# Performance work log

Measured on AMD Instinct MI355X. Metric: run time of the kernel, lower is better.

The kernel has to match this reference:

```python
import jax, jax.numpy as jnp
import numpy as np

N, T, D, H, NH, BS = 4, 4096, 512, 8, 4, 64
DH = D // H                 # head dim = 64
NB = T // BS                # n_buckets = 64
CS = NH * NB                # chunk_size = 256
L = NH * T                  # sorted sequence length per head


def setup_inputs() -> dict:
    key = jax.random.key(0)
    ks = jax.random.split(key, 4)
    x = jax.random.normal(ks[0], (N, T, D), jnp.float32)
    W_Q = jax.random.normal(ks[1], (D, D), jnp.float32) * (D ** -0.5)
    W_V = jax.random.normal(ks[2], (D, D), jnp.float32) * (D ** -0.5)
    b_Q = jnp.zeros((D,), jnp.float32)
    b_V = jnp.zeros((D,), jnp.float32)
    gamma = jnp.ones((D,), jnp.float32)
    beta = jnp.zeros((D,), jnp.float32)
    # per-head random rotations: (dim_head, num_hashes, n_buckets // 2)
    rotations = jax.random.normal(ks[3], (H, DH, NH, NB // 2), jnp.float32)
    return {"x": x, "W_Q": W_Q, "b_Q": b_Q, "W_V": W_V, "b_V": b_V,
            "gamma": gamma, "beta": beta, "rotations": rotations}


def _look_one_back(a):
    # concat each chunk with the previous chunk (wrap-around for chunk 0)
    extra = jnp.concatenate([a[:, -1:], a[:, :-1]], axis=1)
    return jnp.concatenate([a, extra], axis=2)


def _lsh_head(qk, v, rot):
    # qk, v: [N, T, DH]; rot: [DH, NH, NB//2]
    rotated = jnp.einsum('btf,fhi->bhti', qk, rot)               # [N,NH,T,NB//2]
    rotated = jnp.concatenate([rotated, -rotated], axis=-1)       # [N,NH,T,NB]
    buckets = jnp.argmax(rotated, axis=-1)                        # [N,NH,T]
    offsets = (jnp.arange(NH) * NB)[None, :, None]
    buckets = (buckets + offsets).reshape(N, L)                   # [N, NH*T]

    ticker = jnp.broadcast_to(jnp.arange(L)[None, :], (N, L))
    buckets_and_t = T * buckets + (ticker % T)                    # unique keys
    sticker = jnp.argsort(buckets_and_t, axis=-1)                 # sorted ticker ids
    undo_sort = jnp.argsort(sticker, axis=-1)
    st = sticker % T                                              # original positions

    sqk = jnp.take_along_axis(qk, st[..., None], axis=1)          # [N,L,DH]
    sv = jnp.take_along_axis(v, st[..., None], axis=1)

    bq_t = st.reshape(N, CS, -1)                                  # [N,CS,BS]
    bqk = sqk.reshape(N, CS, -1, DH)
    bv = sv.reshape(N, CS, -1, DH)
    bq = bqk
    bk = bqk / (jnp.linalg.norm(bqk, axis=-1, keepdims=True) + 1e-6)

    bk = _look_one_back(bk)                                       # [N,CS,2*BS,DH]
    bv = _look_one_back(bv)
    bkv_t = _look_one_back(bq_t)

    dots = jnp.einsum('bcie,bcje->bcij', bq, bk) * (DH ** -0.5)   # [N,CS,BS,2BS]

    # mask out pairs hashed to different buckets
    q_sb = jnp.take_along_axis(buckets, sticker, axis=1).reshape(N, CS, -1)
    kv_sb = _look_one_back(q_sb)
    dots = jnp.where(q_sb[:, :, :, None] != kv_sb[:, :, None, :], -1e9, dots)
    # down-weight self-attention (same position)
    dots = jnp.where(bq_t[:, :, :, None] == bkv_t[:, :, None, :], -1e-5, dots)

    lse = jax.nn.logsumexp(dots, axis=-1, keepdims=True)
    probs = jnp.exp(dots - lse)
    bo = jnp.einsum('bcij,bcje->bcie', probs, bv)                 # [N,CS,BS,DH]

    so = bo.reshape(N, L, DH)
    slog = lse.reshape(N, L)
    o = jnp.take_along_axis(so, undo_sort[..., None], axis=1)
    logits = jnp.take_along_axis(slog, undo_sort, axis=1)

    o = o.reshape(N, NH, T, DH)
    logits = logits.reshape(N, NH, T, 1)
    pw = jnp.exp(logits - jax.nn.logsumexp(logits, axis=1, keepdims=True))
    return jnp.sum(o * pw, axis=1)                                # [N,T,DH]


def reference(x, W_Q, b_Q, W_V, b_V, gamma, beta, rotations):
    Q = x @ W_Q + b_Q
    V = x @ W_V + b_V
    Qh = Q.reshape(N, T, H, DH).transpose(2, 0, 1, 3)             # [H,N,T,DH]
    Vh = V.reshape(N, T, H, DH).transpose(2, 0, 1, 3)
    outs = jax.vmap(_lsh_head)(Qh, Vh, rotations)                 # [H,N,T,DH]
    out = outs.transpose(1, 2, 0, 3).reshape(N, T, D)
    mu = out.mean(axis=-1, keepdims=True)
    var = out.var(axis=-1, keepdims=True)
    return gamma * (out - mu) / jnp.sqrt(var + 1e-3) + beta
```

## Files before the change

kernel.cpp:

```cpp
#include <hip/hip_runtime.h>
#include <hip/hip_bf16.h>

#define N_ 4
#define T_ 4096
#define D_ 512
#define H_ 8
#define DH_ 64
#define NH_ 4
#define NB_ 64
#define CS_ 256
#define L_ 16384

typedef unsigned short u16;
typedef unsigned int u32;
typedef __attribute__((ext_vector_type(8))) short short8;
typedef __attribute__((ext_vector_type(8))) _Float16 half8;
typedef __attribute__((ext_vector_type(4))) float f32x4;

__device__ __forceinline__ u16 f2bf(float x){
    union { float f; u32 u; } c; c.f = x;
    u32 u = c.u;
    u32 r = (u + 0x7FFFu + ((u >> 16) & 1u)) >> 16;
    return (u16)r;
}
__device__ __forceinline__ float bf2f(u16 b){
    union { u32 u; float f; } c; c.u = ((u32)b) << 16;
    return c.f;
}
__device__ __forceinline__ u16 f2h(float x){
    _Float16 h = (_Float16)x;
    u16 r; __builtin_memcpy(&r, &h, 2); return r;
}

__global__ __launch_bounds__(256) void k_decXf(const float* __restrict__ x,
        u16* __restrict__ xf){
    int i = blockIdx.x * 256 + threadIdx.x;
    float4 v = ((const float4*)x)[i];
    ushort4 o;
    o.x = f2h(v.x); o.y = f2h(v.y); o.z = f2h(v.z); o.w = f2h(v.w);
    ((ushort4*)xf)[i] = o;
}

__global__ __launch_bounds__(256) void k_decWv(const float* __restrict__ Wv,
        u16* __restrict__ wvt){
    __shared__ float tile[32][33];
    const int tid = threadIdx.x;
    const int kt = blockIdx.x * 32, nt = blockIdx.y * 32;
    const int tx = tid & 31, ty = tid >> 5;
    #pragma unroll
    for (int i = 0; i < 4; ++i)
        tile[ty + i * 8][tx] = Wv[(size_t)(kt + ty + i * 8) * 512 + nt + tx];
    __syncthreads();
    #pragma unroll
    for (int i = 0; i < 4; ++i){
        int n = ty + i * 8;
        wvt[(size_t)(nt + n) * 512 + kt + tx] = f2h(tile[tx][n]);
    }
}

__global__ __launch_bounds__(256) void k_q(const float* __restrict__ x,
        const float* __restrict__ Wq, const float* __restrict__ bq,
        float* __restrict__ Q, u16* __restrict__ Qbf, float* __restrict__ qinv){
    __shared__ float sA[16][132];
    __shared__ float sB[16][68];
    const int tid = threadIdx.x;
    const int tx = tid & 15, ty = tid >> 4;
    const int mb = blockIdx.x * 128, nb = blockIdx.y * 64;
    const int h = blockIdx.y;
    float acc[8][4] = {};
    for (int k0 = 0; k0 < 512; k0 += 16){
        #pragma unroll
        for (int i = 0; i < 2; ++i){
            int idx = i * 256 + tid;
            int m = idx >> 2, kq = idx & 3;
            float4 v = *(const float4*)&x[(size_t)(mb + m) * 512 + k0 + kq * 4];
            sA[kq * 4 + 0][m] = v.x;
            sA[kq * 4 + 1][m] = v.y;
            sA[kq * 4 + 2][m] = v.z;
            sA[kq * 4 + 3][m] = v.w;
        }
        {
            int kk = tid >> 4, nq = tid & 15;
            *(float4*)&sB[kk][nq * 4] =
                *(const float4*)&Wq[(size_t)(k0 + kk) * 512 + nb + nq * 4];
        }
        __syncthreads();
        #pragma unroll
        for (int kk = 0; kk < 16; ++kk){
            float a[8], b[4];
            *(float4*)&a[0] = *(const float4*)&sA[kk][ty * 8];
            *(float4*)&a[4] = *(const float4*)&sA[kk][ty * 8 + 4];
            *(float4*)&b[0] = *(const float4*)&sB[kk][tx * 4];
            #pragma unroll
            for (int i = 0; i < 8; ++i)
                #pragma unroll
                for (int j = 0; j < 4; ++j) acc[i][j] += a[i] * b[j];
        }
        __syncthreads();
    }
    float4 bi = *(const float4*)&bq[nb + tx * 4];
    #pragma unroll
    for (int i = 0; i < 8; ++i){
        float o0 = acc[i][0] + bi.x, o1 = acc[i][1] + bi.y;
        float o2 = acc[i][2] + bi.z, o3 = acc[i][3] + bi.w;
        int m = mb + ty * 8 + i;
        float4 o4; o4.x = o0; o4.y = o1; o4.z = o2; o4.w = o3;
        *(float4*)&Q[(size_t)m * 512 + nb + tx * 4] = o4;
        float ss = o0 * o0 + o1 * o1 + o2 * o2 + o3 * o3;
        #pragma unroll
        for (int s = 8; s >= 1; s >>= 1) ss += __shfl_xor(ss, s, 64);
        int n = m >> 12, t = m & (T_ - 1);
        size_t rowb = (size_t)(h * N_ + n) * T_ + t;
        if (tx == 0) qinv[rowb] = 1.f / (sqrtf(ss) + 1e-6f);
        ushort4 ob;
        ob.x = f2bf(o0); ob.y = f2bf(o1); ob.z = f2bf(o2); ob.w = f2bf(o3);
        *(ushort4*)&Qbf[rowb * 64 + tx * 4] = ob;
    }
}

__global__ __launch_bounds__(256) void k_gemmV(const u16* __restrict__ xf,
        const u16* __restrict__ wvt, const float* __restrict__ bv,
        u16* __restrict__ Vbf){
    __shared__ __align__(16) u16 sA[128 * 40];
    __shared__ __align__(16) u16 sB[128 * 40];
    const int tid = threadIdx.x;
    const int mb = blockIdx.x * 128, nb = blockIdx.y * 128;
    const int w = tid >> 6, lane = tid & 63, quad = lane >> 4, cc = lane & 15;
    const int wm = (w & 1) * 64, wn = (w >> 1) * 64;
    f32x4 acc[4][4];
    #pragma unroll
    for (int i = 0; i < 4; ++i)
        #pragma unroll
        for (int j = 0; j < 4; ++j) acc[i][j] = (f32x4){0.f, 0.f, 0.f, 0.f};

    for (int k0 = 0; k0 < 512; k0 += 32){
        #pragma unroll
        for (int i = 0; i < 2; ++i){
            int idx = i * 256 + tid;
            int m = idx >> 2, ks = idx & 3;
            *(short8*)&sA[m * 40 + ks * 8] =
                *(const short8*)&xf[(size_t)(mb + m) * 512 + k0 + ks * 8];
            *(short8*)&sB[m * 40 + ks * 8] =
                *(const short8*)&wvt[(size_t)(nb + m) * 512 + k0 + ks * 8];
        }
        __syncthreads();
        half8 a[4], b[4];
        #pragma unroll
        for (int i = 0; i < 4; ++i){
            a[i] = *(const half8*)&sA[(wm + i * 16 + cc) * 40 + quad * 8];
            b[i] = *(const half8*)&sB[(wn + i * 16 + cc) * 40 + quad * 8];
        }
        #pragma unroll
        for (int i = 0; i < 4; ++i)
            #pragma unroll
            for (int j = 0; j < 4; ++j)
                acc[i][j] = __builtin_amdgcn_mfma_f32_16x16x32_f16(a[i], b[j], acc[i][j], 0, 0, 0);
        __syncthreads();
    }
    #pragma unroll
    for (int i = 0; i < 4; ++i)
        #pragma unroll
        for (int j = 0; j < 4; ++j){
            int c = nb + wn + j * 16 + cc;
            int hh = c >> 6, d = c & 63;
            float bi = bv[c];
            #pragma unroll
            for (int r = 0; r < 4; ++r){
                int m = mb + wm + i * 16 + quad * 4 + r;
                int n = m >> 12, t = m & (T_ - 1);
                Vbf[((size_t)(hh * N_ + n) * T_ + t) * 64 + d] = f2bf(acc[i][j][r] + bi);
            }
        }
}

__global__ __launch_bounds__(256) void k_rot(const float* __restrict__ Q,
        const float* __restrict__ rot, int* __restrict__ buckets){
    const int tb = blockIdx.x * 32;
    const int n = blockIdx.y, h = blockIdx.z;
    const int hn = h * N_ + n;
    __shared__ float Rs[64 * 128];
    __shared__ float Qs[32][64];
    const int tid = threadIdx.x;
    const float* rh = rot + (size_t)h * (64 * 128);
    for (int i = tid; i < 8192; i += 256) Rs[i] = rh[i];
    for (int i = tid; i < 2048; i += 256){
        int t = i >> 6, f = i & 63;
        Qs[t][f] = Q[(size_t)(n * T_ + tb + t) * 512 + h * 64 + f];
    }
    __syncthreads();
    const int tx = tid & 31, tg = tid >> 5;
    float r[4][4] = {};
    for (int f = 0; f < 64; ++f){
        float q0 = Qs[tg * 4 + 0][f], q1 = Qs[tg * 4 + 1][f];
        float q2 = Qs[tg * 4 + 2][f], q3 = Qs[tg * 4 + 3][f];
        #pragma unroll
        for (int jj = 0; jj < 4; ++jj){
            float rv = Rs[f * 128 + jj * 32 + tx];
            r[0][jj] += q0 * rv; r[1][jj] += q1 * rv;
            r[2][jj] += q2 * rv; r[3][jj] += q3 * rv;
        }
    }
    #pragma unroll
    for (int tt = 0; tt < 4; ++tt){
        #pragma unroll
        for (int jj = 0; jj < 4; ++jj){
            float bv = r[tt][jj]; int bi = tx;
            float nv = -bv;
            if (nv > bv){ bv = nv; bi = 32 + tx; }
            #pragma unroll
            for (int m = 16; m >= 1; m >>= 1){
                float ov = __shfl_xor(bv, m, 32);
                int   oi = __shfl_xor(bi, m, 32);
                if (ov > bv || (ov == bv && oi < bi)){ bv = ov; bi = oi; }
            }
            if (tx == 0){
                int t = tb + tg * 4 + tt;
                buckets[(size_t)hn * L_ + jj * T_ + t] = bi + jj * 64;
            }
        }
    }
}

__global__ __launch_bounds__(256) void k_hist(const int* __restrict__ buckets,
        int* __restrict__ hist){
    const int tile = blockIdx.x, hn = blockIdx.y;
    const int tid = threadIdx.x;
    __shared__ int h[256];
    h[tid] = 0;
    __syncthreads();
    int b = buckets[(size_t)hn * L_ + tile * 256 + tid];
    atomicAdd(&h[b], 1);
    __syncthreads();
    hist[((size_t)hn * 64 + tile) * 256 + tid] = h[tid];
}

__global__ __launch_bounds__(256) void k_scan(int* __restrict__ hist,
        int* __restrict__ bucketStart){
    const int hn = blockIdx.x;
    const int b = threadIdx.x;
    int* hh = hist + (size_t)hn * 64 * 256;
    int run = 0;
    for (int tl = 0; tl < 64; ++tl){
        int v = hh[tl * 256 + b];
        hh[tl * 256 + b] = run;
        run += v;
    }
    __shared__ int s[256];
    s[b] = run;
    __syncthreads();
    for (int off = 1; off < 256; off <<= 1){
        int add = (b >= off) ? s[b - off] : 0;
        __syncthreads();
        s[b] += add;
        __syncthreads();
    }
    bucketStart[hn * 256 + b] = s[b] - run;
}

__global__ __launch_bounds__(256) void k_scatter(const int* __restrict__ buckets,
        const int* __restrict__ offs, const int* __restrict__ bucketStart,
        int* __restrict__ sticker){
    const int tile = blockIdx.x, hn = blockIdx.y;
    const int tid = threadIdx.x;
    __shared__ int sb[256];
    const int i = tile * 256 + tid;
    const int b = buckets[(size_t)hn * L_ + i];
    sb[tid] = b;
    __syncthreads();
    int rank = 0;
    #pragma unroll 8
    for (int j = 0; j < 256; ++j){
        int v = sb[j];
        rank += (j < tid && v == b) ? 1 : 0;
    }
    int pos = bucketStart[hn * 256 + b]
            + offs[((size_t)hn * 64 + tile) * 256 + b]
            + rank;
    sticker[(size_t)hn * L_ + pos] = i;
}

__global__ __launch_bounds__(256) void k_attn(const u16* __restrict__ Qbf,
        const u16* __restrict__ Vbf, const float* __restrict__ qinv,
        const int* __restrict__ buckets, const int* __restrict__ sticker,
        u16* __restrict__ o_hash, float* __restrict__ logit_hash){
    const int blk_c = blockIdx.x, n = blockIdx.y, h = blockIdx.z;
    const int hn = h * N_ + n;
    const int tid = threadIdx.x;
    const int w = tid >> 6, lane = tid & 63;
    const int quad = lane >> 4, cc = lane & 15;

    __shared__ __align__(16) u16 sQ[128 * 64];
    __shared__ __align__(16) u16 sVt[64 * 128];
    __shared__ __align__(16) u16 sP[64 * 128];
    __shared__ int s_idx[128], s_buck[128], s_t[128];
    __shared__ float s_inv[128];
    __shared__ float s_lse[64];

    if (tid < 128){
        int cprev = (blk_c + CS_ - 1) & (CS_ - 1);
        int pos = (tid < 64) ? blk_c * 64 + tid : cprev * 64 + (tid - 64);
        int idx = sticker[(size_t)hn * L_ + pos];
        s_idx[tid] = idx;
        s_buck[tid] = buckets[(size_t)hn * L_ + idx];
        int t = idx & (T_ - 1);
        s_t[tid] = t;
        s_inv[tid] = qinv[(size_t)hn * T_ + t];
    }
    __syncthreads();

    const int r0 = tid >> 3, l8 = tid & 7;
    #pragma unroll
    for (int it = 0; it < 4; ++it){
        int r = it * 32 + r0;
        size_t gb = ((size_t)hn * T_ + s_t[r]) * 64 + l8 * 8;
        short8 qv = *(const short8*)&Qbf[gb];
        *(short8*)&sQ[r * 64 + ((l8 ^ (r & 7)) * 8)] = qv;
        short8 vv = *(const short8*)&Vbf[gb];
        #pragma unroll
        for (int i = 0; i < 8; ++i){
            int d = l8 * 8 + i;
            sVt[d * 128 + (((r >> 3) ^ (d & 15)) * 8) + (r & 7)] = (u16)vv[i];
        }
    }
    __syncthreads();

    f32x4 dacc[8];
    #pragma unroll
    for (int j = 0; j < 8; ++j) dacc[j] = (f32x4){0.f, 0.f, 0.f, 0.f};
    const int qrow = w * 16 + cc;
    #pragma unroll
    for (int kc = 0; kc < 2; ++kc){
        short8 afrag = *(const short8*)&sQ[qrow * 64 + (((kc * 4 + quad) ^ (cc & 7)) * 8)];
        #pragma unroll
        for (int kt = 0; kt < 8; ++kt){
            int krow = kt * 16 + cc;
            short8 bfrag = *(const short8*)&sQ[krow * 64 + (((kc * 4 + quad) ^ (cc & 7)) * 8)];
            dacc[kt] = __builtin_amdgcn_mfma_f32_16x16x32_bf16(afrag, bfrag, dacc[kt], 0, 0, 0);
        }
    }

    int bq[4], tq[4];
    #pragma unroll
    for (int r = 0; r < 4; ++r){
        int q = w * 16 + quad * 4 + r;
        bq[r] = s_buck[q]; tq[r] = s_t[q];
    }
    float mrow[4] = {-1e30f, -1e30f, -1e30f, -1e30f};
    #pragma unroll
    for (int kt = 0; kt < 8; ++kt){
        int kk = kt * 16 + cc;
        float inv = s_inv[kk] * 0.125f;
        int bk = s_buck[kk], tk = s_t[kk];
        #pragma unroll
        for (int r = 0; r < 4; ++r){
            float d = dacc[kt][r] * inv;
            if (bk != bq[r]) d = -1e9f;
            if (tk == tq[r]) d = -1e-5f;
            dacc[kt][r] = d;
            mrow[r] = fmaxf(mrow[r], d);
        }
    }
    #pragma unroll
    for (int r = 0; r < 4; ++r)
        #pragma unroll
        for (int m = 8; m >= 1; m >>= 1)
            mrow[r] = fmaxf(mrow[r], __shfl_xor(mrow[r], m, 64));
    float srow[4] = {0.f, 0.f, 0.f, 0.f};
    #pragma unroll
    for (int kt = 0; kt < 8; ++kt)
        #pragma unroll
        for (int r = 0; r < 4; ++r){
            float e = __expf(dacc[kt][r] - mrow[r]);
            dacc[kt][r] = e;
            srow[r] += e;
        }
    #pragma unroll
    for (int r = 0; r < 4; ++r)
        #pragma unroll
        for (int m = 8; m >= 1; m >>= 1)
            srow[r] += __shfl_xor(srow[r], m, 64);
    float lse[4], pscale[4];
    #pragma unroll
    for (int r = 0; r < 4; ++r){
        lse[r] = mrow[r] + __logf(srow[r]);
        pscale[r] = 1.f / srow[r];
    }
    if (cc == 0){
        #pragma unroll
        for (int r = 0; r < 4; ++r) s_lse[w * 16 + quad * 4 + r] = lse[r];
    }

    #pragma unroll
    for (int kt = 0; kt < 8; ++kt){
        int kk = kt * 16 + cc;
        #pragma unroll
        for (int r = 0; r < 4; ++r){
            int q = w * 16 + quad * 4 + r;
            sP[q * 128 + (((kk >> 3) ^ (q & 15)) * 8) + (kk & 7)] =
                f2bf(dacc[kt][r] * pscale[r]);
        }
    }
    __syncthreads();

    f32x4 oacc[4];
    #pragma unroll
    for (int j = 0; j < 4; ++j) oacc[j] = (f32x4){0.f, 0.f, 0.f, 0.f};
    #pragma unroll
    for (int kc = 0; kc < 4; ++kc){
        short8 afrag = *(const short8*)&sP[qrow * 128 + (((kc * 4 + quad) ^ cc) * 8)];
        #pragma unroll
        for (int nt = 0; nt < 4; ++nt){
            int d = nt * 16 + cc;
            short8 bfrag = *(const short8*)&sVt[d * 128 + (((kc * 4 + quad) ^ cc) * 8)];
            oacc[nt] = __builtin_amdgcn_mfma_f32_16x16x32_bf16(afrag, bfrag, oacc[nt], 0, 0, 0);
        }
    }

    #pragma unroll
    for (int r = 0; r < 4; ++r){
        int q = w * 16 + quad * 4 + r;
        int si = s_idx[q];
        int jj = si >> 12; int t = si & (T_ - 1);
        size_t base = ((size_t)(hn * NH_ + jj) * T_ + t) * 64;
        #pragma unroll
        for (int nt = 0; nt < 4; ++nt)
            o_hash[base + nt * 16 + cc] = f2bf(oacc[nt][r]);
    }
    if (tid < 64){
        int si = s_idx[tid]; int jj = si >> 12; int t = si & (T_ - 1);
        logit_hash[(size_t)(hn * NH_ + jj) * T_ + t] = s_lse[tid];
    }
}

__global__ __launch_bounds__(256) void k_comb(const u16* __restrict__ o_hash,
        const float* __restrict__ logit_hash, const float* __restrict__ gamma,
        const float* __restrict__ beta, float* __restrict__ out){
    const int t = blockIdx.x, n = blockIdx.y;
    const int tid = threadIdx.x;
    __shared__ float s_pw[32];
    __shared__ float s_x[512];
    __shared__ float s_red[8];
    __shared__ float s_mu, s_rs;
    if (tid < 32){
        int h = tid >> 2, j = tid & 3;
        s_pw[tid] = logit_hash[(size_t)((h * N_ + n) * NH_ + j) * T_ + t];
    }
    __syncthreads();
    if (tid < 8){
        int h = tid;
        float m = -1e30f;
        #pragma unroll
        for (int j = 0; j < 4; ++j) m = fmaxf(m, s_pw[h * 4 + j]);
        float l = 0.f;
        #pragma unroll
        for (int j = 0; j < 4; ++j) l += __expf(s_pw[h * 4 + j] - m);
        float ls = m + __logf(l);
        #pragma unroll
        for (int j = 0; j < 4; ++j) s_pw[h * 4 + j] = __expf(s_pw[h * 4 + j] - ls);
    }
    __syncthreads();
    float va[2];
    #pragma unroll
    for (int i = 0; i < 2; ++i){
        int cidx = tid + i * 256;
        int h = cidx >> 6, d = cidx & 63;
        size_t base = (size_t)((h * N_ + n) * NH_) * T_ * 64;
        float acc = 0.f;
        #pragma unroll
        for (int j = 0; j < 4; ++j)
            acc += s_pw[h * 4 + j] * bf2f(o_hash[base + ((size_t)j * T_ + t) * 64 + d]);
        s_x[cidx] = acc; va[i] = acc;
    }
    float s1 = va[0] + va[1];
    float s2 = va[0] * va[0] + va[1] * va[1];
    #pragma unroll
    for (int m = 32; m >= 1; m >>= 1){
        s1 += __shfl_xor(s1, m, 64);
        s2 += __shfl_xor(s2, m, 64);
    }
    const int lane = tid & 63, w = tid >> 6;
    if (lane == 0){ s_red[w] = s1; s_red[4 + w] = s2; }
    __syncthreads();
    if (tid == 0){
        float S1 = s_red[0] + s_red[1] + s_red[2] + s_red[3];
        float S2 = s_red[4] + s_red[5] + s_red[6] + s_red[7];
        float mu = S1 / 512.f;
        float var = S2 / 512.f - mu * mu;
        s_mu = mu; s_rs = 1.f / sqrtf(var + 1e-3f);
    }
    __syncthreads();
    #pragma unroll
    for (int i = 0; i < 2; ++i){
        int cidx = tid + i * 256;
        out[((size_t)(n * T_ + t)) * 512 + cidx] =
            gamma[cidx] * (s_x[cidx] - s_mu) * s_rs + beta[cidx];
    }
}

extern "C" void kernel_launch(void* const* d_in, const int* in_sizes, int n_in,
                              void* d_out, int out_size, void* d_ws, size_t ws_size,
                              hipStream_t stream){
    const float* x     = (const float*)d_in[0];
    const float* Wq    = (const float*)d_in[1];
    const float* bq    = (const float*)d_in[2];
    const float* Wv    = (const float*)d_in[3];
    const float* bv    = (const float*)d_in[4];
    const float* gamma = (const float*)d_in[5];
    const float* beta  = (const float*)d_in[6];
    const float* rot   = (const float*)d_in[7];
    char* ws = (char*)d_ws;
    float* Q        = (float*)(ws + 0);
    u16*   o_hash   = (u16*)  (ws + 0);
    u16*   Qbf      = (u16*)  (ws + 67108864);
    u16*   Vbf      = (u16*)  (ws + 83886080);
    float* qinv     = (float*)(ws + 100663296);
    int*   buckets  = (int*)  (ws + 101187584);
    int*   sticker  = (int*)  (ws + 103284736);
    float* logit    = (float*)(ws + 105381888);
    int*   hist     = (int*)  (ws + 107479040);
    int*   bstart   = (int*)  (ws + 109576192);
    u16*   xf       = (u16*)  (ws + 109608960);
    u16*   wvt      = (u16*)  (ws + 126386176);

    hipLaunchKernelGGL(k_decXf,   dim3(8192),       dim3(256), 0, stream,
                       x, xf);
    hipLaunchKernelGGL(k_decWv,   dim3(16, 16),     dim3(256), 0, stream,
                       Wv, wvt);
    hipLaunchKernelGGL(k_gemmV,   dim3(128, 4),     dim3(256), 0, stream,
                       xf, wvt, bv, Vbf);
    hipLaunchKernelGGL(k_q,       dim3(128, 8),     dim3(256), 0, stream,
                       x, Wq, bq, Q, Qbf, qinv);
    hipLaunchKernelGGL(k_rot,     dim3(128, 4, 8),  dim3(256), 0, stream,
                       Q, rot, buckets);
    hipLaunchKernelGGL(k_hist,    dim3(64, 32),     dim3(256), 0, stream,
                       buckets, hist);
    hipLaunchKernelGGL(k_scan,    dim3(32),         dim3(256), 0, stream,
                       hist, bstart);
    hipLaunchKernelGGL(k_scatter, dim3(64, 32),     dim3(256), 0, stream,
                       buckets, hist, bstart, sticker);
    hipLaunchKernelGGL(k_attn,    dim3(256, 4, 8),  dim3(256), 0, stream,
                       Qbf, Vbf, qinv, buckets, sticker, o_hash, logit);
    hipLaunchKernelGGL(k_comb,    dim3(4096, 4),    dim3(256), 0, stream,
                       o_hash, logit, gamma, beta, (float*)d_out);
}
```

Measured before the change: 444.0 us.

## Widen fp32 Q projection tile to two heads with packed FMA and prefetch

The fp32 Q GEMM now computes a 128x128 output tile per block, covering two heads, instead of 128x64. Each thread does 8x8 outputs using v_pk_fma_f32 inline asm. Global loads for the next k-slice are prefetched into registers while the current slice is computed. The aim is more reuse per shared-memory load, double the FMA throughput through the packed instructions, and hidden global-load latency. In exchange the block count halves (512 blocks), register pressure rises, and the inline asm constrains the scheduler.

```diff
diff --git a/kernel.cpp b/kernel.cpp
--- a/kernel.cpp
+++ b/kernel.cpp
@@ -16,6 +16,7 @@
 typedef __attribute__((ext_vector_type(8))) short short8;
 typedef __attribute__((ext_vector_type(8))) _Float16 half8;
 typedef __attribute__((ext_vector_type(4))) float f32x4;
+typedef __attribute__((ext_vector_type(2))) float f32x2;
 
 __device__ __forceinline__ u16 f2bf(float x){
     union { float f; u32 u; } c; c.f = x;
@@ -31,6 +32,13 @@
     _Float16 h = (_Float16)x;
     u16 r; __builtin_memcpy(&r, &h, 2); return r;
 }
+
+#define PK_LO(acc, a, b) \
+    asm("v_pk_fma_f32 %0, %1, %2, %0 op_sel:[0,0,0] op_sel_hi:[0,1,1]" \
+        : "+v"(acc) : "v"(a), "v"(b))
+#define PK_HI(acc, a, b) \
+    asm("v_pk_fma_f32 %0, %1, %2, %0 op_sel:[1,0,0] op_sel_hi:[1,1,1]" \
+        : "+v"(acc) : "v"(a), "v"(b))
 
 __global__ __launch_bounds__(256) void k_decXf(const float* __restrict__ x,
         u16* __restrict__ xf){
@@ -62,59 +70,102 @@
         const float* __restrict__ Wq, const float* __restrict__ bq,
         float* __restrict__ Q, u16* __restrict__ Qbf, float* __restrict__ qinv){
     __shared__ float sA[16][132];
-    __shared__ float sB[16][68];
+    __shared__ float sB[16][132];
     const int tid = threadIdx.x;
     const int tx = tid & 15, ty = tid >> 4;
-    const int mb = blockIdx.x * 128, nb = blockIdx.y * 64;
-    const int h = blockIdx.y;
-    float acc[8][4] = {};
+    const int mb = blockIdx.x * 128, nb = blockIdx.y * 128;
+
+    f32x2 acc2[8][4];
+    #pragma unroll
+    for (int i = 0; i < 8; ++i)
+        #pragma unroll
+        for (int j = 0; j < 4; ++j) acc2[i][j] = (f32x2){0.f, 0.f};
+
+    const int mA = tid >> 2, kA = (tid & 3) * 4;
+    const int kB = tid >> 5, cB = (tid & 31) * 4;
+    const float* xp0 = &x[(size_t)(mb + mA) * 512 + kA];
+    const float* xp1 = xp0 + (size_t)64 * 512;
+    const float* wp0 = &Wq[(size_t)kB * 512 + nb + cB];
+    const float* wp1 = wp0 + (size_t)8 * 512;
+
+    float4 pa0 = *(const float4*)(xp0);
+    float4 pa1 = *(const float4*)(xp1);
+    float4 pb0 = *(const float4*)(wp0);
+    float4 pb1 = *(const float4*)(wp1);
+
     for (int k0 = 0; k0 < 512; k0 += 16){
-        #pragma unroll
-        for (int i = 0; i < 2; ++i){
-            int idx = i * 256 + tid;
-            int m = idx >> 2, kq = idx & 3;
-            float4 v = *(const float4*)&x[(size_t)(mb + m) * 512 + k0 + kq * 4];
-            sA[kq * 4 + 0][m] = v.x;
-            sA[kq * 4 + 1][m] = v.y;
-            sA[kq * 4 + 2][m] = v.z;
-            sA[kq * 4 + 3][m] = v.w;
-        }
-        {
-            int kk = tid >> 4, nq = tid & 15;
-            *(float4*)&sB[kk][nq * 4] =
-                *(const float4*)&Wq[(size_t)(k0 + kk) * 512 + nb + nq * 4];
-        }
         __syncthreads();
+        sA[kA + 0][mA] = pa0.x; sA[kA + 1][mA] = pa0.y;
+        sA[kA + 2][mA] = pa0.z; sA[kA + 3][mA] = pa0.w;
+        sA[kA + 0][64 + mA] = pa1.x; sA[kA + 1][64 + mA] = pa1.y;
+        sA[kA + 2][64 + mA] = pa1.z; sA[kA + 3][64 + mA] = pa1.w;
+        *(float4*)&sB[kB][cB] = pb0;
+        *(float4*)&sB[kB + 8][cB] = pb1;
+        if (k0 < 496){
+            pa0 = *(const float4*)(xp0 + k0 + 16);
+            pa1 = *(const float4*)(xp1 + k0 + 16);
+            pb0 = *(const float4*)(wp0 + (size_t)(k0 + 16) * 512);
+            pb1 = *(const float4*)(wp1 + (size_t)(k0 + 16) * 512);
+        }
+        __syncthreads();
         #pragma unroll
         for (int kk = 0; kk < 16; ++kk){
-            float a[8], b[4];
-            *(float4*)&a[0] = *(const float4*)&sA[kk][ty * 8];
-            *(float4*)&a[4] = *(const float4*)&sA[kk][ty * 8 + 4];
-            *(float4*)&b[0] = *(const float4*)&sB[kk][tx * 4];
+            float4 va0 = *(const float4*)&sA[kk][ty * 8];
+            float4 va1 = *(const float4*)&sA[kk][ty * 8 + 4];
+            float4 vb0 = *(const float4*)&sB[kk][tx * 4];
+            float4 vb1 = *(const float4*)&sB[kk][64 + tx * 4];
+            f32x2 a2[4], b2[4];
+            a2[0] = (f32x2){va0.x, va0.y}; a2[1] = (f32x2){va0.z, va0.w};
+            a2[2] = (f32x2){va1.x, va1.y}; a2[3] = (f32x2){va1.z, va1.w};
+            b2[0] = (f32x2){vb0.x, vb0.y}; b2[1] = (f32x2){vb0.z, vb0.w};
+            b2[2] = (f32x2){vb1.x, vb1.y}; b2[3] = (f32x2){vb1.z, vb1.w};
             #pragma unroll
-            for (int i = 0; i < 8; ++i)
+            for (int i = 0; i < 8; ++i){
                 #pragma unroll
-                for (int j = 0; j < 4; ++j) acc[i][j] += a[i] * b[j];
-        }
-        __syncthreads();
-    }
-    float4 bi = *(const float4*)&bq[nb + tx * 4];
+                for (int jp = 0; jp < 4; ++jp){
+                    if (i & 1) { PK_HI(acc2[i][jp], a2[i >> 1], b2[jp]); }
+                    else       { PK_LO(acc2[i][jp], a2[i >> 1], b2[jp]); }
+                }
+            }
+        }
+    }
+
+    float4 vb0 = *(const float4*)&bq[nb + tx * 4];
+    float4 vb1 = *(const float4*)&bq[nb + 64 + tx * 4];
+    f32x2 bi[4];
+    bi[0] = (f32x2){vb0.x, vb0.y}; bi[1] = (f32x2){vb0.z, vb0.w};
+    bi[2] = (f32x2){vb1.x, vb1.y}; bi[3] = (f32x2){vb1.z, vb1.w};
+    const int h0 = blockIdx.y * 2;
     #pragma unroll
     for (int i = 0; i < 8; ++i){
-        float o0 = acc[i][0] + bi.x, o1 = acc[i][1] + bi.y;
-        float o2 = acc[i][2] + bi.z, o3 = acc[i][3] + bi.w;
+        f32x2 o[4];
+        #pragma unroll
+        for (int jp = 0; jp < 4; ++jp) o[jp] = acc2[i][jp] + bi[jp];
         int m = mb + ty * 8 + i;
-        float4 o4; o4.x = o0; o4.y = o1; o4.z = o2; o4.w = o3;
-        *(float4*)&Q[(size_t)m * 512 + nb + tx * 4] = o4;
-        float ss = o0 * o0 + o1 * o1 + o2 * o2 + o3 * o3;
-        #pragma unroll
-        for (int s = 8; s >= 1; s >>= 1) ss += __shfl_xor(ss, s, 64);
         int n = m >> 12, t = m & (T_ - 1);
-        size_t rowb = (size_t)(h * N_ + n) * T_ + t;
-        if (tx == 0) qinv[rowb] = 1.f / (sqrtf(ss) + 1e-6f);
-        ushort4 ob;
-        ob.x = f2bf(o0); ob.y = f2bf(o1); ob.z = f2bf(o2); ob.w = f2bf(o3);
-        *(ushort4*)&Qbf[rowb * 64 + tx * 4] = ob;
+        float4 q0, q1;
+        q0.x = o[0].x; q0.y = o[0].y; q0.z = o[1].x; q0.w = o[1].y;
+        q1.x = o[2].x; q1.y = o[2].y; q1.z = o[3].x; q1.w = o[3].y;
+        *(float4*)&Q[(size_t)m * 512 + nb + tx * 4] = q0;
+        *(float4*)&Q[(size_t)m * 512 + nb + 64 + tx * 4] = q1;
+        float ssA = q0.x * q0.x + q0.y * q0.y + q0.z * q0.z + q0.w * q0.w;
+        float ssB = q1.x * q1.x + q1.y * q1.y + q1.z * q1.z + q1.w * q1.w;
+        #pragma unroll
+        for (int s = 8; s >= 1; s >>= 1){
+            ssA += __shfl_xor(ssA, s, 64);
+            ssB += __shfl_xor(ssB, s, 64);
+        }
+        size_t rowbA = (size_t)(h0 * N_ + n) * T_ + t;
+        size_t rowbB = rowbA + (size_t)N_ * T_;
+        if (tx == 0){
+            qinv[rowbA] = 1.f / (sqrtf(ssA) + 1e-6f);
+            qinv[rowbB] = 1.f / (sqrtf(ssB) + 1e-6f);
+        }
+        ushort4 qa, qb;
+        qa.x = f2bf(q0.x); qa.y = f2bf(q0.y); qa.z = f2bf(q0.z); qa.w = f2bf(q0.w);
+        qb.x = f2bf(q1.x); qb.y = f2bf(q1.y); qb.z = f2bf(q1.z); qb.w = f2bf(q1.w);
+        *(ushort4*)&Qbf[rowbA * 64 + tx * 4] = qa;
+        *(ushort4*)&Qbf[rowbB * 64 + tx * 4] = qb;
     }
 }
 
@@ -528,7 +579,7 @@
                        Wv, wvt);
     hipLaunchKernelGGL(k_gemmV,   dim3(128, 4),     dim3(256), 0, stream,
                        xf, wvt, bv, Vbf);
-    hipLaunchKernelGGL(k_q,       dim3(128, 8),     dim3(256), 0, stream,
+    hipLaunchKernelGGL(k_q,       dim3(128, 4),     dim3(256), 0, stream,
                        x, Wq, bq, Q, Qbf, qinv);
     hipLaunchKernelGGL(k_rot,     dim3(128, 4, 8),  dim3(256), 0, stream,
                        Q, rot, buckets);
```

After: 419.7 us. -5.5%, faster.

## Use packed FP32 FMA in Q projection and rotation kernels with double-buffered tiles

Applied to the files above, without the earlier changes.

The Q-projection GEMM is rewritten with 512-thread blocks covering 128x128 tiles. It double-buffers LDS, register-prefetches the next k-slice, drops the second barrier, and issues v_pk_fma_f32 through inline asm. The rotation kernel relays out the rotation matrix in LDS so each thread reads float4 values, and it also uses packed FMAs over pairs of f. The aim is to double FP32 FMA throughput and cut LDS instructions and barriers. The cost is higher register pressure in k_q and inline asm that the compiler cannot schedule around.

```diff
diff --git a/kernel.cpp b/kernel.cpp
--- a/kernel.cpp
+++ b/kernel.cpp
@@ -16,6 +16,7 @@
 typedef __attribute__((ext_vector_type(8))) short short8;
 typedef __attribute__((ext_vector_type(8))) _Float16 half8;
 typedef __attribute__((ext_vector_type(4))) float f32x4;
+typedef __attribute__((ext_vector_type(2))) float f32x2;
 
 __device__ __forceinline__ u16 f2bf(float x){
     union { float f; u32 u; } c; c.f = x;
@@ -31,6 +32,13 @@
     _Float16 h = (_Float16)x;
     u16 r; __builtin_memcpy(&r, &h, 2); return r;
 }
+
+#define PK_LO(acc, a, b) \
+    asm("v_pk_fma_f32 %0, %1, %2, %0 op_sel:[0,0,0] op_sel_hi:[0,1,1]" \
+        : "+v"(acc) : "v"(a), "v"(b))
+#define PK_HI(acc, a, b) \
+    asm("v_pk_fma_f32 %0, %1, %2, %0 op_sel:[1,0,0] op_sel_hi:[1,1,1]" \
+        : "+v"(acc) : "v"(a), "v"(b))
 
 __global__ __launch_bounds__(256) void k_decXf(const float* __restrict__ x,
         u16* __restrict__ xf){
@@ -58,63 +66,83 @@
     }
 }
 
-__global__ __launch_bounds__(256) void k_q(const float* __restrict__ x,
+__global__ __launch_bounds__(512, 4) void k_q(const float* __restrict__ x,
         const float* __restrict__ Wq, const float* __restrict__ bq,
         float* __restrict__ Q, u16* __restrict__ Qbf, float* __restrict__ qinv){
-    __shared__ float sA[16][132];
-    __shared__ float sB[16][68];
-    const int tid = threadIdx.x;
-    const int tx = tid & 15, ty = tid >> 4;
-    const int mb = blockIdx.x * 128, nb = blockIdx.y * 64;
-    const int h = blockIdx.y;
-    float acc[8][4] = {};
+    __shared__ float sA[2][16][132];
+    __shared__ float sB[2][16][132];
+    const int tid = threadIdx.x;
+    const int tx = tid & 31, ty = tid >> 5;
+    const int mb = blockIdx.x * 128, nb = blockIdx.y * 128;
+
+    f32x2 acc2[8][2];
+    #pragma unroll
+    for (int i = 0; i < 8; ++i){
+        acc2[i][0] = (f32x2){0.f, 0.f};
+        acc2[i][1] = (f32x2){0.f, 0.f};
+    }
+
+    const int mA = tid >> 2, kA = (tid & 3) * 4;
+    const int kB = tid >> 5, cB = (tid & 31) * 4;
+    const float* xp = &x[(size_t)(mb + mA) * 512 + kA];
+    const float* wp = &Wq[(size_t)kB * 512 + nb + cB];
+
+    float4 pa = *(const float4*)xp;
+    float4 pb = *(const float4*)wp;
+
     for (int k0 = 0; k0 < 512; k0 += 16){
-        #pragma unroll
-        for (int i = 0; i < 2; ++i){
-            int idx = i * 256 + tid;
-            int m = idx >> 2, kq = idx & 3;
-            float4 v = *(const float4*)&x[(size_t)(mb + m) * 512 + k0 + kq * 4];
-            sA[kq * 4 + 0][m] = v.x;
-            sA[kq * 4 + 1][m] = v.y;
-            sA[kq * 4 + 2][m] = v.z;
-            sA[kq * 4 + 3][m] = v.w;
-        }
-        {
-            int kk = tid >> 4, nq = tid & 15;
-            *(float4*)&sB[kk][nq * 4] =
-                *(const float4*)&Wq[(size_t)(k0 + kk) * 512 + nb + nq * 4];
-        }
+        const int p = (k0 >> 4) & 1;
+        sA[p][kA + 0][mA] = pa.x; sA[p][kA + 1][mA] = pa.y;
+        sA[p][kA + 2][mA] = pa.z; sA[p][kA + 3][mA] = pa.w;
+        *(float4*)&sB[p][kB][cB] = pb;
         __syncthreads();
+        if (k0 < 496){
+            pa = *(const float4*)(xp + k0 + 16);
+            pb = *(const float4*)(wp + (size_t)(k0 + 16) * 512);
+        }
         #pragma unroll
         for (int kk = 0; kk < 16; ++kk){
-            float a[8], b[4];
-            *(float4*)&a[0] = *(const float4*)&sA[kk][ty * 8];
-            *(float4*)&a[4] = *(const float4*)&sA[kk][ty * 8 + 4];
-            *(float4*)&b[0] = *(const float4*)&sB[kk][tx * 4];
+            float4 va0 = *(const float4*)&sA[p][kk][ty * 8];
+            float4 va1 = *(const float4*)&sA[p][kk][ty * 8 + 4];
+            float4 vb  = *(const float4*)&sB[p][kk][tx * 4];
+            f32x2 a2[4], b2[2];
+            a2[0] = (f32x2){va0.x, va0.y}; a2[1] = (f32x2){va0.z, va0.w};
+            a2[2] = (f32x2){va1.x, va1.y}; a2[3] = (f32x2){va1.z, va1.w};
+            b2[0] = (f32x2){vb.x, vb.y};   b2[1] = (f32x2){vb.z, vb.w};
             #pragma unroll
-            for (int i = 0; i < 8; ++i)
-                #pragma unroll
-                for (int j = 0; j < 4; ++j) acc[i][j] += a[i] * b[j];
-        }
-        __syncthreads();
-    }
-    float4 bi = *(const float4*)&bq[nb + tx * 4];
+            for (int i = 0; i < 8; ++i){
+                if (i & 1){
+                    PK_HI(acc2[i][0], a2[i >> 1], b2[0]);
+                    PK_HI(acc2[i][1], a2[i >> 1], b2[1]);
+                } else {
+                    PK_LO(acc2[i][0], a2[i >> 1], b2[0]);
+                    PK_LO(acc2[i][1], a2[i >> 1], b2[1]);
+                }
+            }
+        }
+    }
+
+    float4 vbq = *(const float4*)&bq[nb + tx * 4];
+    const int h = blockIdx.y * 2 + (tx >> 4);
+    const int d0 = (tx & 15) * 4;
     #pragma unroll
     for (int i = 0; i < 8; ++i){
-        float o0 = acc[i][0] + bi.x, o1 = acc[i][1] + bi.y;
-        float o2 = acc[i][2] + bi.z, o3 = acc[i][3] + bi.w;
+        float o0 = acc2[i][0].x + vbq.x;
+        float o1 = acc2[i][0].y + vbq.y;
+        float o2 = acc2[i][1].x + vbq.z;
+        float o3 = acc2[i][1].y + vbq.w;
         int m = mb + ty * 8 + i;
-        float4 o4; o4.x = o0; o4.y = o1; o4.z = o2; o4.w = o3;
-        *(float4*)&Q[(size_t)m * 512 + nb + tx * 4] = o4;
+        int n = m >> 12, t = m & (T_ - 1);
+        float4 q4; q4.x = o0; q4.y = o1; q4.z = o2; q4.w = o3;
+        *(float4*)&Q[(size_t)m * 512 + nb + tx * 4] = q4;
         float ss = o0 * o0 + o1 * o1 + o2 * o2 + o3 * o3;
         #pragma unroll
         for (int s = 8; s >= 1; s >>= 1) ss += __shfl_xor(ss, s, 64);
-        int n = m >> 12, t = m & (T_ - 1);
         size_t rowb = (size_t)(h * N_ + n) * T_ + t;
-        if (tx == 0) qinv[rowb] = 1.f / (sqrtf(ss) + 1e-6f);
-        ushort4 ob;
-        ob.x = f2bf(o0); ob.y = f2bf(o1); ob.z = f2bf(o2); ob.w = f2bf(o3);
-        *(ushort4*)&Qbf[rowb * 64 + tx * 4] = ob;
+        if ((tx & 15) == 0) qinv[rowb] = 1.f / (sqrtf(ss) + 1e-6f);
+        ushort4 qb4;
+        qb4.x = f2bf(o0); qb4.y = f2bf(o1); qb4.z = f2bf(o2); qb4.w = f2bf(o3);
+        *(ushort4*)&Qbf[rowb * 64 + d0] = qb4;
     }
 }
 
@@ -182,29 +210,46 @@
     __shared__ float Qs[32][64];
     const int tid = threadIdx.x;
     const float* rh = rot + (size_t)h * (64 * 128);
-    for (int i = tid; i < 8192; i += 256) Rs[i] = rh[i];
+    for (int idx = tid; idx < 8192; idx += 256){
+        int f = idx >> 7, rem = idx & 127, jj = rem >> 5, i2 = rem & 31;
+        Rs[f * 128 + i2 * 4 + jj] = rh[idx];
+    }
     for (int i = tid; i < 2048; i += 256){
         int t = i >> 6, f = i & 63;
         Qs[t][f] = Q[(size_t)(n * T_ + tb + t) * 512 + h * 64 + f];
     }
     __syncthreads();
     const int tx = tid & 31, tg = tid >> 5;
-    float r[4][4] = {};
-    for (int f = 0; f < 64; ++f){
-        float q0 = Qs[tg * 4 + 0][f], q1 = Qs[tg * 4 + 1][f];
-        float q2 = Qs[tg * 4 + 2][f], q3 = Qs[tg * 4 + 3][f];
+    f32x2 r2[4][2];
+    #pragma unroll
+    for (int tt = 0; tt < 4; ++tt){
+        r2[tt][0] = (f32x2){0.f, 0.f};
+        r2[tt][1] = (f32x2){0.f, 0.f};
+    }
+    for (int f = 0; f < 64; f += 2){
+        f32x2 qf[4];
+        #pragma unroll
+        for (int tt = 0; tt < 4; ++tt)
+            qf[tt] = *(const f32x2*)&Qs[tg * 4 + tt][f];
+        float4 rv0 = *(const float4*)&Rs[f * 128 + tx * 4];
+        float4 rv1 = *(const float4*)&Rs[(f + 1) * 128 + tx * 4];
+        f32x2 b0[2], b1[2];
+        b0[0] = (f32x2){rv0.x, rv0.y}; b0[1] = (f32x2){rv0.z, rv0.w};
+        b1[0] = (f32x2){rv1.x, rv1.y}; b1[1] = (f32x2){rv1.z, rv1.w};
+        #pragma unroll
+        for (int tt = 0; tt < 4; ++tt){
+            PK_LO(r2[tt][0], qf[tt], b0[0]);
+            PK_LO(r2[tt][1], qf[tt], b0[1]);
+            PK_HI(r2[tt][0], qf[tt], b1[0]);
+            PK_HI(r2[tt][1], qf[tt], b1[1]);
+        }
+    }
+    #pragma unroll
+    for (int tt = 0; tt < 4; ++tt){
         #pragma unroll
         for (int jj = 0; jj < 4; ++jj){
-            float rv = Rs[f * 128 + jj * 32 + tx];
-            r[0][jj] += q0 * rv; r[1][jj] += q1 * rv;
-            r[2][jj] += q2 * rv; r[3][jj] += q3 * rv;
-        }
-    }
-    #pragma unroll
-    for (int tt = 0; tt < 4; ++tt){
-        #pragma unroll
-        for (int jj = 0; jj < 4; ++jj){
-            float bv = r[tt][jj]; int bi = tx;
+            float rval = (jj < 2) ? r2[tt][0][jj] : r2[tt][1][jj - 2];
+            float bv = rval; int bi = tx;
             float nv = -bv;
             if (nv > bv){ bv = nv; bi = 32 + tx; }
             #pragma unroll
@@ -528,7 +573,7 @@
                        Wv, wvt);
     hipLaunchKernelGGL(k_gemmV,   dim3(128, 4),     dim3(256), 0, stream,
                        xf, wvt, bv, Vbf);
-    hipLaunchKernelGGL(k_q,       dim3(128, 8),     dim3(256), 0, stream,
+    hipLaunchKernelGGL(k_q,       dim3(128, 4),     dim3(512), 0, stream,
                        x, Wq, bq, Q, Qbf, qinv);
     hipLaunchKernelGGL(k_rot,     dim3(128, 4, 8),  dim3(256), 0, stream,
                        Q, rot, buckets);
```

Result: faster. 400.2 us (-9.9%).
